# Optimization experiments

Measured on AMD Instinct MI355X. Metric: run time of the kernel, lower is better.

Reference implementation:

```python
import jax, jax.numpy as jnp
import numpy as np

EMBED_DIM = 512

def _equalized_linear(x, W):
    # StyleGAN equalized LR: effective weight = W / sqrt(fan_in); out = x @ W_eff.T
    c = 1.0 / np.sqrt(W.shape[1])
    return jnp.einsum('bnd,ed->bne', x, W) * c

def setup_inputs() -> dict:
    key = jax.random.key(0)
    ks = jax.random.split(key, 6)
    B, N, D = 16, 2048, 512
    return {
        'q': jax.random.normal(ks[0], (B, N, D), dtype=jnp.float32),
        'k': jax.random.normal(ks[1], (B, N, D), dtype=jnp.float32),
        'v': jax.random.normal(ks[2], (B, N, D), dtype=jnp.float32),
        'Wq': jax.random.normal(ks[3], (EMBED_DIM, D), dtype=jnp.float32),
        'Wk': jax.random.normal(ks[4], (EMBED_DIM, D), dtype=jnp.float32),
        'Wv': jax.random.normal(ks[5], (EMBED_DIM, D), dtype=jnp.float32),
    }

def reference(q, k, v, Wq, Wk, Wv):
    scale = EMBED_DIM ** (-0.5)
    qp = _equalized_linear(q, Wq)  # [B,Nq,E]
    kp = _equalized_linear(k, Wk)  # [B,Nk,E]
    vp = _equalized_linear(v, Wv)  # [B,Nk,E]
    dots = jnp.einsum('bqe,bke->bqk', qp, kp) * scale  # [B,Nq,Nk]
    attn = jax.nn.softmax(dots, axis=-1)
    out = jnp.einsum('bqk,bke->bqe', attn, vp)  # [B,Nq,E]
    return (out, attn)
```

## Files before the change

kernel.cpp:

```cpp
#include <hip/hip_runtime.h>
#include <hip/hip_bf16.h>

typedef __attribute__((ext_vector_type(8))) short short8;
typedef __attribute__((ext_vector_type(4))) float floatx4;

#define LDP 72
#define TP  136
#define PP  40

#define ATTN_OFF ((size_t)16 * 2048 * 512)

__device__ __forceinline__ unsigned short f2bf(float f) {
    union { __hip_bfloat16 h; unsigned short u; } cv;
    cv.h = __float2bfloat16(f);
    return cv.u;
}

__device__ __forceinline__ uint2 f4_to_bf4(float x, float y, float z, float w) {
    uint2 r;
    r.x = (unsigned)f2bf(x) | ((unsigned)f2bf(y) << 16);
    r.y = (unsigned)f2bf(z) | ((unsigned)f2bf(w) << 16);
    return r;
}

__global__ __launch_bounds__(256, 2)
void proj_kernel(const float* __restrict__ q, const float* __restrict__ k,
                 const float* __restrict__ v, const float* __restrict__ wq,
                 const float* __restrict__ wk, const float* __restrict__ wv,
                 unsigned short* __restrict__ qp, unsigned short* __restrict__ kp,
                 unsigned short* __restrict__ vpT)
{
    const int mat = blockIdx.z;
    const float* __restrict__ x = (mat == 0) ? q : (mat == 1) ? k : v;
    const float* __restrict__ w = (mat == 0) ? wq : (mat == 1) ? wk : wv;
    const float scale = (mat == 0) ? (1.0f / 512.0f) : 0.044194173824159216f;

    const int m0 = blockIdx.x * 128;
    const int n0 = blockIdx.y * 128;

    __shared__ __align__(16) unsigned short sm[2 * 128 * LDP];
    unsigned short* lds_a = sm;
    unsigned short* lds_b = sm + 128 * LDP;
    unsigned short* lds_t = sm;

    const int t = threadIdx.x;
    const int wave = t >> 6, ln = t & 15, qd = (t >> 4) & 3;
    const int wm = wave >> 1, wn = wave & 1;

    floatx4 acc[4][4];
    for (int mi = 0; mi < 4; ++mi)
        for (int ni = 0; ni < 4; ++ni)
            acc[mi][ni] = (floatx4){0.f, 0.f, 0.f, 0.f};

    for (int kb = 0; kb < 512; kb += 64) {
        for (int i = 0; i < 8; ++i) {
            int lin = t + 256 * i;
            int row = lin >> 4, c4 = lin & 15;
            const float4 a4 = *(const float4*)&x[(size_t)(m0 + row) * 512 + kb + c4 * 4];
            *(uint2*)&lds_a[row * LDP + c4 * 4] = f4_to_bf4(a4.x, a4.y, a4.z, a4.w);
            const float4 b4 = *(const float4*)&w[(size_t)(n0 + row) * 512 + kb + c4 * 4];
            *(uint2*)&lds_b[row * LDP + c4 * 4] = f4_to_bf4(b4.x, b4.y, b4.z, b4.w);
        }
        __syncthreads();
        for (int kk = 0; kk < 2; ++kk) {
            short8 af[4], bg[4];
            for (int mi = 0; mi < 4; ++mi)
                af[mi] = *(const short8*)&lds_a[(wm * 64 + mi * 16 + ln) * LDP + kk * 32 + qd * 8];
            for (int ni = 0; ni < 4; ++ni)
                bg[ni] = *(const short8*)&lds_b[(wn * 64 + ni * 16 + ln) * LDP + kk * 32 + qd * 8];
            for (int mi = 0; mi < 4; ++mi)
                for (int ni = 0; ni < 4; ++ni)
                    acc[mi][ni] = __builtin_amdgcn_mfma_f32_16x16x32_bf16(
                        af[mi], bg[ni], acc[mi][ni], 0, 0, 0);
        }
        __syncthreads();
    }

    for (int mi = 0; mi < 4; ++mi)
        for (int ni = 0; ni < 4; ++ni)
            for (int r = 0; r < 4; ++r) {
                float val = acc[mi][ni][r] * scale;
                int row = wm * 64 + mi * 16 + qd * 4 + r;
                int col = wn * 64 + ni * 16 + ln;
                if (mat == 2) lds_t[col * TP + row] = f2bf(val);
                else          lds_t[row * TP + col] = f2bf(val);
            }
    __syncthreads();
    if (mat < 2) {
        unsigned short* dst = (mat == 0) ? qp : kp;
        for (int i = 0; i < 8; ++i) {
            int lin = t + 256 * i;
            int row = lin >> 4, c8 = lin & 15;
            *(uint4*)&dst[(size_t)(m0 + row) * 512 + n0 + c8 * 8] =
                *(const uint4*)&lds_t[row * TP + c8 * 8];
        }
    } else {
        int b = m0 >> 11;
        int tloc = m0 & 2047;
        for (int i = 0; i < 8; ++i) {
            int lin = t + 256 * i;
            int row = lin >> 4, c8 = lin & 15;
            *(uint4*)&vpT[(size_t)b * 512 * 2048 + (size_t)(n0 + row) * 2048 + tloc + c8 * 8] =
                *(const uint4*)&lds_t[row * TP + c8 * 8];
        }
    }
}

__global__ __launch_bounds__(256, 2)
void dots_kernel(const unsigned short* __restrict__ qp, const unsigned short* __restrict__ kp,
                 float* __restrict__ attn, float* __restrict__ lsum)
{
    const int b = blockIdx.z;
    const int row0 = blockIdx.y * 128;
    const int col0 = blockIdx.x * 128;

    __shared__ __align__(16) unsigned short sm[2 * 128 * LDP];
    unsigned short* lds_a = sm;
    unsigned short* lds_b = sm + 128 * LDP;
    __shared__ float lds_l[128];

    const int t = threadIdx.x;
    const int wave = t >> 6, ln = t & 15, qd = (t >> 4) & 3;
    const int wm = wave >> 1, wn = wave & 1;

    if (t < 128) lds_l[t] = 0.f;

    const unsigned short* arow = qp + (size_t)(b * 2048 + row0) * 512;
    const unsigned short* brow = kp + (size_t)(b * 2048 + col0) * 512;

    floatx4 acc[4][4];
    for (int mi = 0; mi < 4; ++mi)
        for (int ni = 0; ni < 4; ++ni)
            acc[mi][ni] = (floatx4){0.f, 0.f, 0.f, 0.f};

    for (int kb = 0; kb < 512; kb += 64) {
        for (int i = 0; i < 4; ++i) {
            int lin = t + 256 * i;
            int row = lin >> 3, c8 = lin & 7;
            *(uint4*)&lds_a[row * LDP + c8 * 8] = *(const uint4*)&arow[(size_t)row * 512 + kb + c8 * 8];
            *(uint4*)&lds_b[row * LDP + c8 * 8] = *(const uint4*)&brow[(size_t)row * 512 + kb + c8 * 8];
        }
        __syncthreads();
        for (int kk = 0; kk < 2; ++kk) {
            short8 af[4], bg[4];
            for (int mi = 0; mi < 4; ++mi)
                af[mi] = *(const short8*)&lds_a[(wm * 64 + mi * 16 + ln) * LDP + kk * 32 + qd * 8];
            for (int ni = 0; ni < 4; ++ni)
                bg[ni] = *(const short8*)&lds_b[(wn * 64 + ni * 16 + ln) * LDP + kk * 32 + qd * 8];
            for (int mi = 0; mi < 4; ++mi)
                for (int ni = 0; ni < 4; ++ni)
                    acc[mi][ni] = __builtin_amdgcn_mfma_f32_16x16x32_bf16(
                        af[mi], bg[ni], acc[mi][ni], 0, 0, 0);
        }
        __syncthreads();
    }

    float* attnb = attn + (size_t)(b * 2048 + row0) * 2048 + col0;
    for (int mi = 0; mi < 4; ++mi) {
        float s[4] = {0.f, 0.f, 0.f, 0.f};
        for (int ni = 0; ni < 4; ++ni) {
            int colL = wn * 64 + ni * 16 + ln;
            for (int r = 0; r < 4; ++r) {
                float p = __expf(acc[mi][ni][r]);
                int rowL = wm * 64 + mi * 16 + qd * 4 + r;
                attnb[(size_t)rowL * 2048 + colL] = p;
                s[r] += p;
            }
        }
        for (int r = 0; r < 4; ++r) {
            float vv = s[r];
            vv += __shfl_xor(vv, 1);
            vv += __shfl_xor(vv, 2);
            vv += __shfl_xor(vv, 4);
            vv += __shfl_xor(vv, 8);
            if (ln == 0) atomicAdd(&lds_l[wm * 64 + mi * 16 + qd * 4 + r], vv);
        }
    }
    __syncthreads();
    if (t < 128) atomicAdd(&lsum[b * 2048 + row0 + t], lds_l[t]);
}

__global__ __launch_bounds__(512, 4)
void out_kernel(const unsigned short* __restrict__ vpT, float* __restrict__ attn,
                const float* __restrict__ lsum, float* __restrict__ out)
{
    const int b  = blockIdx.x;
    const int r0 = blockIdx.y * 64;

    __shared__ __align__(16) unsigned short p_lds[2][64 * PP];

    const int t = threadIdx.x;
    const int wave = t >> 6, ln = t & 15, qd = (t >> 4) & 3;
    const int wn = wave;

    const int prow = t >> 3;
    const int pcol = (t & 7) * 4;
    const float il = 1.0f / lsum[b * 2048 + r0 + prow];

    float* pbase = attn + (size_t)(b * 2048 + r0 + prow) * 2048 + pcol;
    const unsigned short* vb = vpT + (size_t)b * 512 * 2048;

    floatx4 acc[4][4];
    #pragma unroll
    for (int mi = 0; mi < 4; ++mi)
        #pragma unroll
        for (int ni = 0; ni < 4; ++ni)
            acc[mi][ni] = (floatx4){0.f, 0.f, 0.f, 0.f};

    {
        float4 pa = *(const float4*)(pbase);
        pa.x *= il; pa.y *= il; pa.z *= il; pa.w *= il;
        *(float4*)(pbase) = pa;
        uint2 pk = f4_to_bf4(pa.x, pa.y, pa.z, pa.w);
        *(uint2*)&p_lds[0][prow * PP + pcol] = pk;
    }

    for (int i = 0; i < 64; ++i) {
        const int kc = i * 32;
        const int buf = i & 1;
        __syncthreads();

        float4 pa;
        if (i < 63) pa = *(const float4*)(pbase + kc + 32);

        short8 bg[4];
        #pragma unroll
        for (int ni = 0; ni < 4; ++ni)
            bg[ni] = *(const short8*)&vb[(size_t)(wn * 64 + ni * 16 + ln) * 2048 + kc + qd * 8];

        short8 af[4];
        #pragma unroll
        for (int mi = 0; mi < 4; ++mi)
            af[mi] = *(const short8*)&p_lds[buf][(mi * 16 + ln) * PP + qd * 8];

        #pragma unroll
        for (int ni = 0; ni < 4; ++ni)
            #pragma unroll
            for (int mi = 0; mi < 4; ++mi)
                acc[mi][ni] = __builtin_amdgcn_mfma_f32_16x16x32_bf16(
                    af[mi], bg[ni], acc[mi][ni], 0, 0, 0);

        if (i < 63) {
            pa.x *= il; pa.y *= il; pa.z *= il; pa.w *= il;
            *(float4*)(pbase + kc + 32) = pa;
            uint2 pk = f4_to_bf4(pa.x, pa.y, pa.z, pa.w);
            *(uint2*)&p_lds[buf ^ 1][prow * PP + pcol] = pk;
        }
    }

    float* outb = out + (size_t)(b * 2048 + r0) * 512;
    #pragma unroll
    for (int mi = 0; mi < 4; ++mi)
        #pragma unroll
        for (int ni = 0; ni < 4; ++ni) {
            int col = wn * 64 + ni * 16 + ln;
            #pragma unroll
            for (int r = 0; r < 4; ++r) {
                int row = mi * 16 + qd * 4 + r;
                outb[(size_t)row * 512 + col] = acc[mi][ni][r];
            }
        }
}

extern "C" void kernel_launch(void* const* d_in, const int* in_sizes, int n_in,
                              void* d_out, int out_size, void* d_ws, size_t ws_size,
                              hipStream_t stream) {
    const float* q  = (const float*)d_in[0];
    const float* k  = (const float*)d_in[1];
    const float* v  = (const float*)d_in[2];
    const float* wq = (const float*)d_in[3];
    const float* wk = (const float*)d_in[4];
    const float* wv = (const float*)d_in[5];

    unsigned short* qp  = (unsigned short*)d_ws;
    unsigned short* kp  = qp + (size_t)32768 * 512;
    unsigned short* vpT = kp + (size_t)32768 * 512;
    float* lsum = (float*)(vpT + (size_t)16 * 512 * 2048);

    float* out  = (float*)d_out;
    float* attn = out + ATTN_OFF;

    hipMemsetAsync(lsum, 0, (size_t)16 * 2048 * sizeof(float), stream);

    proj_kernel<<<dim3(256, 4, 3), 256, 0, stream>>>(q, k, v, wq, wk, wv, qp, kp, vpT);
    dots_kernel<<<dim3(16, 16, 16), 256, 0, stream>>>(qp, kp, attn, lsum);
    out_kernel<<<dim3(16, 32), 512, 0, stream>>>(vpT, attn, lsum, out);
}
```

Measured before the change: 902.5 us.

## Retile out_kernel so each wave owns 16 rows, with chunked V layout

The V projection is now stored in a chunked [batch][token/32][embed][32] layout, so each 32-token k-step reads one contiguous 32 KB slab. out_kernel is rewritten so each wave handles 16 query rows across all 512 output columns. Each wave loads, normalizes and writes back its own attn fragment directly into MFMA A registers, which removes the LDS staging and the per-iteration __syncthreads. The block now covers 128 rows, halving the grid, and holds 32 accumulator tiles per lane. This raises register pressure and lowers occupancy (launch bounds 512,2). Each wave also reloads the full V slab from global/L2 instead of sharing it, trading more V traffic for no barriers.

```diff
diff --git a/kernel.cpp b/kernel.cpp
--- a/kernel.cpp
+++ b/kernel.cpp
@@ -6,7 +6,6 @@
 
 #define LDP 72
 #define TP  136
-#define PP  40
 
 #define ATTN_OFF ((size_t)16 * 2048 * 512)
 
@@ -21,6 +20,14 @@
     r.x = (unsigned)f2bf(x) | ((unsigned)f2bf(y) << 16);
     r.y = (unsigned)f2bf(z) | ((unsigned)f2bf(w) << 16);
     return r;
+}
+
+__device__ __forceinline__ short8 f8_to_bf8(float4 a, float4 b) {
+    union { uint4 u; short8 s; } cv;
+    uint2 lo = f4_to_bf4(a.x, a.y, a.z, a.w);
+    uint2 hi = f4_to_bf4(b.x, b.y, b.z, b.w);
+    cv.u.x = lo.x; cv.u.y = lo.y; cv.u.z = hi.x; cv.u.w = hi.y;
+    return cv.s;
 }
 
 __global__ __launch_bounds__(256, 2)
@@ -100,7 +107,9 @@
         for (int i = 0; i < 8; ++i) {
             int lin = t + 256 * i;
             int row = lin >> 4, c8 = lin & 15;
-            *(uint4*)&vpT[(size_t)b * 512 * 2048 + (size_t)(n0 + row) * 2048 + tloc + c8 * 8] =
+            int tok = tloc + c8 * 8;
+            *(uint4*)&vpT[(size_t)b * 1048576 + (size_t)(tok >> 5) * 16384
+                          + (size_t)(n0 + row) * 32 + (tok & 31)] =
                 *(const uint4*)&lds_t[row * TP + c8 * 8];
         }
     }
@@ -180,86 +189,69 @@
     if (t < 128) atomicAdd(&lsum[b * 2048 + row0 + t], lds_l[t]);
 }
 
-__global__ __launch_bounds__(512, 4)
+__global__ __launch_bounds__(512, 2)
 void out_kernel(const unsigned short* __restrict__ vpT, float* __restrict__ attn,
                 const float* __restrict__ lsum, float* __restrict__ out)
 {
     const int b  = blockIdx.x;
-    const int r0 = blockIdx.y * 64;
-
-    __shared__ __align__(16) unsigned short p_lds[2][64 * PP];
+    const int r0 = blockIdx.y * 128;
 
     const int t = threadIdx.x;
-    const int wave = t >> 6, ln = t & 15, qd = (t >> 4) & 3;
-    const int wn = wave;
-
-    const int prow = t >> 3;
-    const int pcol = (t & 7) * 4;
-    const float il = 1.0f / lsum[b * 2048 + r0 + prow];
-
-    float* pbase = attn + (size_t)(b * 2048 + r0 + prow) * 2048 + pcol;
-    const unsigned short* vb = vpT + (size_t)b * 512 * 2048;
-
-    floatx4 acc[4][4];
+    const int w = t >> 6, ln = t & 15, qd = (t >> 4) & 3;
+
+    const int row = r0 + w * 16 + ln;
+    const float il = 1.0f / lsum[b * 2048 + row];
+
+    float* prow = attn + ((size_t)b * 2048 + row) * 2048;
+    const unsigned short* vb = vpT + (size_t)b * 1048576;
+
+    floatx4 acc[32];
     #pragma unroll
-    for (int mi = 0; mi < 4; ++mi)
-        #pragma unroll
-        for (int ni = 0; ni < 4; ++ni)
-            acc[mi][ni] = (floatx4){0.f, 0.f, 0.f, 0.f};
-
-    {
-        float4 pa = *(const float4*)(pbase);
-        pa.x *= il; pa.y *= il; pa.z *= il; pa.w *= il;
-        *(float4*)(pbase) = pa;
-        uint2 pk = f4_to_bf4(pa.x, pa.y, pa.z, pa.w);
-        *(uint2*)&p_lds[0][prow * PP + pcol] = pk;
-    }
+    for (int ni = 0; ni < 32; ++ni)
+        acc[ni] = (floatx4){0.f, 0.f, 0.f, 0.f};
+
+    float4 a0 = *(const float4*)(prow + qd * 8);
+    float4 a1 = *(const float4*)(prow + qd * 8 + 4);
 
     for (int i = 0; i < 64; ++i) {
         const int kc = i * 32;
-        const int buf = i & 1;
-        __syncthreads();
-
-        float4 pa;
-        if (i < 63) pa = *(const float4*)(pbase + kc + 32);
-
-        short8 bg[4];
+
+        float4 n0, n1;
+        if (i < 63) {
+            n0 = *(const float4*)(prow + kc + 32 + qd * 8);
+            n1 = *(const float4*)(prow + kc + 36 + qd * 8);
+        }
+
+        a0.x *= il; a0.y *= il; a0.z *= il; a0.w *= il;
+        a1.x *= il; a1.y *= il; a1.z *= il; a1.w *= il;
+        *(float4*)(prow + kc + qd * 8)     = a0;
+        *(float4*)(prow + kc + qd * 8 + 4) = a1;
+        short8 af = f8_to_bf8(a0, a1);
+
+        const unsigned short* vk = vb + (size_t)i * 16384;
         #pragma unroll
-        for (int ni = 0; ni < 4; ++ni)
-            bg[ni] = *(const short8*)&vb[(size_t)(wn * 64 + ni * 16 + ln) * 2048 + kc + qd * 8];
-
-        short8 af[4];
+        for (int g = 0; g < 8; ++g) {
+            short8 b0 = *(const short8*)&vk[((g * 4 + 0) * 16 + ln) * 32 + qd * 8];
+            short8 b1 = *(const short8*)&vk[((g * 4 + 1) * 16 + ln) * 32 + qd * 8];
+            short8 b2 = *(const short8*)&vk[((g * 4 + 2) * 16 + ln) * 32 + qd * 8];
+            short8 b3 = *(const short8*)&vk[((g * 4 + 3) * 16 + ln) * 32 + qd * 8];
+            acc[g * 4 + 0] = __builtin_amdgcn_mfma_f32_16x16x32_bf16(af, b0, acc[g * 4 + 0], 0, 0, 0);
+            acc[g * 4 + 1] = __builtin_amdgcn_mfma_f32_16x16x32_bf16(af, b1, acc[g * 4 + 1], 0, 0, 0);
+            acc[g * 4 + 2] = __builtin_amdgcn_mfma_f32_16x16x32_bf16(af, b2, acc[g * 4 + 2], 0, 0, 0);
+            acc[g * 4 + 3] = __builtin_amdgcn_mfma_f32_16x16x32_bf16(af, b3, acc[g * 4 + 3], 0, 0, 0);
+        }
+
+        if (i < 63) { a0 = n0; a1 = n1; }
+    }
+
+    float* outb = out + ((size_t)b * 2048 + r0 + w * 16) * 512;
+    #pragma unroll
+    for (int ni = 0; ni < 32; ++ni) {
         #pragma unroll
-        for (int mi = 0; mi < 4; ++mi)
-            af[mi] = *(const short8*)&p_lds[buf][(mi * 16 + ln) * PP + qd * 8];
-
-        #pragma unroll
-        for (int ni = 0; ni < 4; ++ni)
-            #pragma unroll
-            for (int mi = 0; mi < 4; ++mi)
-                acc[mi][ni] = __builtin_amdgcn_mfma_f32_16x16x32_bf16(
-                    af[mi], bg[ni], acc[mi][ni], 0, 0, 0);
-
-        if (i < 63) {
-            pa.x *= il; pa.y *= il; pa.z *= il; pa.w *= il;
-            *(float4*)(pbase + kc + 32) = pa;
-            uint2 pk = f4_to_bf4(pa.x, pa.y, pa.z, pa.w);
-            *(uint2*)&p_lds[buf ^ 1][prow * PP + pcol] = pk;
-        }
-    }
-
-    float* outb = out + (size_t)(b * 2048 + r0) * 512;
-    #pragma unroll
-    for (int mi = 0; mi < 4; ++mi)
-        #pragma unroll
-        for (int ni = 0; ni < 4; ++ni) {
-            int col = wn * 64 + ni * 16 + ln;
-            #pragma unroll
-            for (int r = 0; r < 4; ++r) {
-                int row = mi * 16 + qd * 4 + r;
-                outb[(size_t)row * 512 + col] = acc[mi][ni][r];
-            }
-        }
+        for (int r = 0; r < 4; ++r) {
+            outb[(size_t)(qd * 4 + r) * 512 + ni * 16 + ln] = acc[ni][r];
+        }
+    }
 }
 
 extern "C" void kernel_launch(void* const* d_in, const int* in_sizes, int n_in,
@@ -284,5 +276,5 @@
 
     proj_kernel<<<dim3(256, 4, 3), 256, 0, stream>>>(q, k, v, wq, wk, wv, qp, kp, vpT);
     dots_kernel<<<dim3(16, 16, 16), 256, 0, stream>>>(qp, kp, attn, lsum);
-    out_kernel<<<dim3(16, 32), 512, 0, stream>>>(vpT, attn, lsum, out);
-}
+    out_kernel<<<dim3(16, 16), 512, 0, stream>>>(vpT, attn, lsum, out);
+}
```

Result: slower. 1.034 ms (+14.6%).
